# Performance work log

Hardware: AMD Instinct MI355X
Metric: run time of the kernel (lower is better)

## Reference

```python
import jax, jax.numpy as jnp
import numpy as np

DN = ('NCH', 'OIH', 'NCH')  # conv dimension numbers: [batch, channel, length]

def setup_inputs() -> dict:
    key = jax.random.key(0)
    ks = jax.random.split(key, 8)
    B, S, L, D, F, V = 16, 64, 128, 512, 256, 30000
    return {
        'text': jax.random.randint(ks[0], (B, S, L), 0, V),
        'embed': jax.random.normal(ks[1], (V, D), dtype=jnp.float32),
        'w3': jax.random.normal(ks[2], (F, D, 3), dtype=jnp.float32) * 0.05,
        'b3': jax.random.normal(ks[3], (F,), dtype=jnp.float32) * 0.05,
        'w4': jax.random.normal(ks[4], (F, D, 4), dtype=jnp.float32) * 0.05,
        'b4': jax.random.normal(ks[5], (F,), dtype=jnp.float32) * 0.05,
        'w5': jax.random.normal(ks[6], (F, D, 5), dtype=jnp.float32) * 0.05,
        'b5': jax.random.normal(ks[7], (F,), dtype=jnp.float32) * 0.05,
    }

def reference(text, embed, w3, b3, w4, b4, w5, b5):
    B, S, L = text.shape
    # Embed tokens, flatten episodes x utterances into one batch, channels-first.
    x = embed[text]                                   # [B, S, L, D]
    x = x.reshape(B * S, L, -1).transpose(0, 2, 1)    # [BS, D, L]
    outs = []
    for w, b in ((w3, b3), (w4, b4), (w5, b5)):
        y = jax.lax.conv_general_dilated(x, w, (1,), 'VALID', dimension_numbers=DN)
        # max-over-time pooling (valid conv -> length L-K+1)
        outs.append(jnp.max(y + b[None, :, None], axis=2))  # [BS, F]
    out = jax.nn.relu(jnp.concatenate(outs, axis=1))  # [BS, 3F]
    return out.reshape(B, S, -1)
```

## Files before the change

### kernel.cpp

```cpp
#include <hip/hip_runtime.h>
#include <hip/hip_bf16.h>


typedef __bf16 bf16x8 __attribute__((ext_vector_type(8)));
typedef float f32x4 __attribute__((ext_vector_type(4)));

#define XROWS 132
#define XELEMS ((size_t)1024 * XROWS * 512)
#define SLAB_STRIDE 520
#define SLAB_ROWS 133
#define SLAB_BYTES (SLAB_ROWS * SLAB_STRIDE * 2)
#define WQ_ELEMS 1572864

__device__ __forceinline__ void async16(const void* g, void* l) {
    __builtin_amdgcn_global_load_lds(
        (const __attribute__((address_space(1))) void*)g,
        (__attribute__((address_space(3))) void*)l, 16, 0, 0);
}

__global__ void pack_x_kernel(const int* __restrict__ text,
                              const float* __restrict__ embed,
                              __bf16* __restrict__ x) {
    const int tid  = threadIdx.x;
    const int rr   = blockIdx.x * 4 + (tid >> 6);
    const int lane = tid & 63;
    const int bs   = rr / XROWS;
    const int t    = rr - bs * XROWS;
    __bf16* dst = x + (size_t)rr * 512 + lane * 8;
    bf16x8 o = {};
    if (t < 128) {
        const int token = text[bs * 128 + t];
        const float* src = embed + (size_t)token * 512 + lane * 8;
        const float4 v0 = *(const float4*)(src);
        const float4 v1 = *(const float4*)(src + 4);
        o[0] = (__bf16)v0.x; o[1] = (__bf16)v0.y;
        o[2] = (__bf16)v0.z; o[3] = (__bf16)v0.w;
        o[4] = (__bf16)v1.x; o[5] = (__bf16)v1.y;
        o[6] = (__bf16)v1.z; o[7] = (__bf16)v1.w;
    }
    *(bf16x8*)dst = o;
}

__global__ void pack_w_kernel(const float* __restrict__ w3,
                              const float* __restrict__ w4,
                              const float* __restrict__ w5,
                              __bf16* __restrict__ wq) {
    const int t    = blockIdx.x * 256 + threadIdx.x;
    const int g    = t >> 6;
    const int lane = t & 63;
    int rel, Kw; const float* w;
    if (g < 768)       { rel = g;        Kw = 3; w = w3; }
    else if (g < 1792) { rel = g - 768;  Kw = 4; w = w4; }
    else               { rel = g - 1792; Kw = 5; w = w5; }
    const int kq  = rel >> 4;
    const int n16 = rel & 15;
    const int f   = n16 * 16 + (lane & 15);
    const int k0  = kq * 32 + (lane >> 4) * 8;
    const int tap = k0 >> 9;
    const int d0  = k0 & 511;
    const float* src = w + ((size_t)f * 512 + d0) * Kw + tap;
    bf16x8 o;
#pragma unroll
    for (int j = 0; j < 8; ++j) o[j] = (__bf16)src[j * Kw];
    *(bf16x8*)(wq + (size_t)t * 8) = o;
}

__global__ __launch_bounds__(512, 2) void conv_gemm_kernel(
        const __bf16* __restrict__ x,
        const __bf16* __restrict__ wq,
        const float* __restrict__ b3,
        const float* __restrict__ b4,
        const float* __restrict__ b5,
        float* __restrict__ out) {
    extern __shared__ __bf16 slab[];

    const int tid  = threadIdx.x;
    const int wave = tid >> 6;
    const int lane = tid & 63;

    const int lin = blockIdx.x;
    const int xcd = lin & 7;
    const int idx = lin >> 3;
    const int bsh = idx / 3;
    const int c   = idx - bsh * 3;
    const int bs  = bsh * 8 + xcd;
    const int KW  = 3 + c;
    const int nkq = KW << 4;
    const int cbase = (c == 0) ? 0 : (c == 1) ? 393216 : 917504;

    const __bf16* xb = x + (size_t)bs * (XROWS * 512);

    for (int r = wave; r < XROWS; r += 8)
        async16(xb + r * 512 + lane * 8, &slab[r * SLAB_STRIDE]);
    __syncthreads();

    const int wm = wave & 1, wn = wave >> 1;
    const int lm = lane & 15, lk = lane >> 4;

    const __bf16* ap = slab + (wm * 64 + lm) * SLAB_STRIDE + lk * 8;
    const __bf16* bp = wq + cbase + (size_t)(wn * 4) * 512 + lane * 8;

    f32x4 acc[4][4];
#pragma unroll
    for (int i = 0; i < 4; ++i)
#pragma unroll
        for (int j = 0; j < 4; ++j) acc[i][j] = (f32x4){0.f, 0.f, 0.f, 0.f};

    bf16x8 A2[2][4], B4[4][4];

    auto loadB = [&](bf16x8* d, int kb) {
        const __bf16* p = bp + (size_t)kb * 8192;
        d[0] = *(const bf16x8*)(p);
        d[1] = *(const bf16x8*)(p + 512);
        d[2] = *(const bf16x8*)(p + 1024);
        d[3] = *(const bf16x8*)(p + 1536);
    };
    auto mfma16 = [&](const bf16x8* a, const bf16x8* b) {
#pragma unroll
        for (int mt = 0; mt < 4; ++mt)
#pragma unroll
            for (int nt = 0; nt < 4; ++nt)
                acc[mt][nt] = __builtin_amdgcn_mfma_f32_16x16x32_bf16(
                    a[mt], b[nt], acc[mt][nt], 0, 0, 0);
    };

    loadB(B4[0], 0); loadB(B4[1], 1); loadB(B4[2], 2); loadB(B4[3], 3);
#pragma unroll
    for (int mt = 0; mt < 4; ++mt) {
        A2[0][mt] = *(const bf16x8*)(ap + mt * (16 * SLAB_STRIDE));
        A2[1][mt] = *(const bf16x8*)(ap + 32 + mt * (16 * SLAB_STRIDE));
    }

    for (int tap = 0; tap < KW; ++tap) {
        const int kq0 = tap << 4;
#pragma unroll
        for (int q = 0; q < 16; ++q) {
            mfma16(A2[q & 1], B4[q & 3]);
            {
                const int off = (q + 2 < 16) ? (q + 2) * 32
                                             : SLAB_STRIDE + (q - 14) * 32;
#pragma unroll
                for (int mt = 0; mt < 4; ++mt)
                    A2[q & 1][mt] = *(const bf16x8*)
                        (ap + off + mt * (16 * SLAB_STRIDE));
            }
            {
                int kb = kq0 + q + 4;
                kb = (kb < nkq) ? kb : (nkq - 1);
                loadB(B4[q & 3], kb);
            }
        }
        ap += SLAB_STRIDE;
    }

    const int Tv = 126 - c;
    float cmax[4];
#pragma unroll
    for (int nt = 0; nt < 4; ++nt) {
        float mx = -3.0e38f;
#pragma unroll
        for (int mt = 0; mt < 4; ++mt) {
            const int mb = wm * 64 + mt * 16 + lk * 4;
#pragma unroll
            for (int r = 0; r < 4; ++r) {
                const float v = acc[mt][nt][r];
                if (mb + r < Tv) mx = fmaxf(mx, v);
            }
        }
        mx = fmaxf(mx, __shfl_xor(mx, 16, 64));
        mx = fmaxf(mx, __shfl_xor(mx, 32, 64));
        cmax[nt] = mx;
    }
    __syncthreads();
    float* red = (float*)slab;
    if (lk == 0) {
#pragma unroll
        for (int nt = 0; nt < 4; ++nt)
            red[wm * 256 + wn * 64 + nt * 16 + lm] = cmax[nt];
    }
    __syncthreads();
    if (tid < 256) {
        const float* bias = (c == 0) ? b3 : (c == 1) ? b4 : b5;
        float v = fmaxf(red[tid], red[256 + tid]) + bias[tid];
        out[(size_t)bs * 768 + c * 256 + tid] = fmaxf(v, 0.f);
    }
}

extern "C" void kernel_launch(void* const* d_in, const int* in_sizes, int n_in,
                              void* d_out, int out_size, void* d_ws, size_t ws_size,
                              hipStream_t stream) {
    const int*   text  = (const int*)d_in[0];
    const float* embed = (const float*)d_in[1];
    const float* w3    = (const float*)d_in[2];
    const float* b3    = (const float*)d_in[3];
    const float* w4    = (const float*)d_in[4];
    const float* b4    = (const float*)d_in[5];
    const float* w5    = (const float*)d_in[6];
    const float* b5    = (const float*)d_in[7];
    float* out = (float*)d_out;

    __bf16* x  = (__bf16*)d_ws;
    __bf16* wq = x + XELEMS;

    (void)hipFuncSetAttribute((const void*)conv_gemm_kernel,
                              hipFuncAttributeMaxDynamicSharedMemorySize,
                              SLAB_BYTES);

    pack_x_kernel<<<1024 * XROWS / 4, 256, 0, stream>>>(text, embed, x);
    pack_w_kernel<<<768, 256, 0, stream>>>(w3, w4, w5, wq);
    conv_gemm_kernel<<<3072, 512, SLAB_BYTES, stream>>>(x, wq, b3, b4, b5, out);
}
```

Baseline: 514.5 us.

## Fuse embedding gather into conv GEMM with half-depth swizzled LDS slab

Removes the separate pack_x kernel and its bf16 workspace round-trip, so each conv block gathers and converts its own embedding rows straight into LDS. The D dimension is processed in two halves of 256, which shrinks the LDS slab to 132x512 bytes and uses an XOR swizzle in place of padding to avoid bank conflicts. Blocks grow to 1024 threads with a 4x4 wave grid and half the accumulators per wave. In exchange, each embedding row is re-gathered from fp32 three times (once per filter width), and the gather for the second half serialises behind a barrier instead of overlapping with compute.

```diff
diff --git a/kernel.cpp b/kernel.cpp
--- a/kernel.cpp
+++ b/kernel.cpp
@@ -5,41 +5,10 @@
 typedef __bf16 bf16x8 __attribute__((ext_vector_type(8)));
 typedef float f32x4 __attribute__((ext_vector_type(4)));
 
-#define XROWS 132
-#define XELEMS ((size_t)1024 * XROWS * 512)
-#define SLAB_STRIDE 520
-#define SLAB_ROWS 133
-#define SLAB_BYTES (SLAB_ROWS * SLAB_STRIDE * 2)
+#define ROWS 132
+#define ROWB 512
+#define SLAB_BYTES (ROWS * ROWB)
 #define WQ_ELEMS 1572864
-
-__device__ __forceinline__ void async16(const void* g, void* l) {
-    __builtin_amdgcn_global_load_lds(
-        (const __attribute__((address_space(1))) void*)g,
-        (__attribute__((address_space(3))) void*)l, 16, 0, 0);
-}
-
-__global__ void pack_x_kernel(const int* __restrict__ text,
-                              const float* __restrict__ embed,
-                              __bf16* __restrict__ x) {
-    const int tid  = threadIdx.x;
-    const int rr   = blockIdx.x * 4 + (tid >> 6);
-    const int lane = tid & 63;
-    const int bs   = rr / XROWS;
-    const int t    = rr - bs * XROWS;
-    __bf16* dst = x + (size_t)rr * 512 + lane * 8;
-    bf16x8 o = {};
-    if (t < 128) {
-        const int token = text[bs * 128 + t];
-        const float* src = embed + (size_t)token * 512 + lane * 8;
-        const float4 v0 = *(const float4*)(src);
-        const float4 v1 = *(const float4*)(src + 4);
-        o[0] = (__bf16)v0.x; o[1] = (__bf16)v0.y;
-        o[2] = (__bf16)v0.z; o[3] = (__bf16)v0.w;
-        o[4] = (__bf16)v1.x; o[5] = (__bf16)v1.y;
-        o[6] = (__bf16)v1.z; o[7] = (__bf16)v1.w;
-    }
-    *(bf16x8*)dst = o;
-}
 
 __global__ void pack_w_kernel(const float* __restrict__ w3,
                               const float* __restrict__ w4,
@@ -65,14 +34,15 @@
     *(bf16x8*)(wq + (size_t)t * 8) = o;
 }
 
-__global__ __launch_bounds__(512, 2) void conv_gemm_kernel(
-        const __bf16* __restrict__ x,
+__global__ __launch_bounds__(1024, 4) void conv_gemm_kernel(
+        const int* __restrict__ text,
+        const float* __restrict__ embed,
         const __bf16* __restrict__ wq,
         const float* __restrict__ b3,
         const float* __restrict__ b4,
         const float* __restrict__ b5,
         float* __restrict__ out) {
-    extern __shared__ __bf16 slab[];
+    extern __shared__ char slab[];
 
     const int tid  = threadIdx.x;
     const int wave = tid >> 6;
@@ -85,29 +55,21 @@
     const int c   = idx - bsh * 3;
     const int bs  = bsh * 8 + xcd;
     const int KW  = 3 + c;
-    const int nkq = KW << 4;
-    const int cbase = (c == 0) ? 0 : (c == 1) ? 393216 : 917504;
-
-    const __bf16* xb = x + (size_t)bs * (XROWS * 512);
-
-    for (int r = wave; r < XROWS; r += 8)
-        async16(xb + r * 512 + lane * 8, &slab[r * SLAB_STRIDE]);
-    __syncthreads();
-
-    const int wm = wave & 1, wn = wave >> 1;
+    const size_t cbase = (c == 0) ? 0 : (c == 1) ? 393216 : 917504;
+
+    const int wm = wave & 3, wn = wave >> 2;
     const int lm = lane & 15, lk = lane >> 4;
-
-    const __bf16* ap = slab + (wm * 64 + lm) * SLAB_STRIDE + lk * 8;
+    const int ls = lane & 31, lh = lane >> 5;
+
     const __bf16* bp = wq + cbase + (size_t)(wn * 4) * 512 + lane * 8;
 
-    f32x4 acc[4][4];
-#pragma unroll
-    for (int i = 0; i < 4; ++i)
+    f32x4 acc[2][4];
+#pragma unroll
+    for (int i = 0; i < 2; ++i)
 #pragma unroll
         for (int j = 0; j < 4; ++j) acc[i][j] = (f32x4){0.f, 0.f, 0.f, 0.f};
 
-    bf16x8 A2[2][4], B4[4][4];
-
+    bf16x8 B4[2][4];
     auto loadB = [&](bf16x8* d, int kb) {
         const __bf16* p = bp + (size_t)kb * 8192;
         d[0] = *(const bf16x8*)(p);
@@ -115,42 +77,68 @@
         d[2] = *(const bf16x8*)(p + 1024);
         d[3] = *(const bf16x8*)(p + 1536);
     };
-    auto mfma16 = [&](const bf16x8* a, const bf16x8* b) {
-#pragma unroll
-        for (int mt = 0; mt < 4; ++mt)
-#pragma unroll
-            for (int nt = 0; nt < 4; ++nt)
-                acc[mt][nt] = __builtin_amdgcn_mfma_f32_16x16x32_bf16(
-                    a[mt], b[nt], acc[mt][nt], 0, 0, 0);
+    auto mfma8 = [&](const bf16x8 a0, const bf16x8 a1, const bf16x8* b) {
+#pragma unroll
+        for (int nt = 0; nt < 4; ++nt)
+            acc[0][nt] = __builtin_amdgcn_mfma_f32_16x16x32_bf16(
+                a0, b[nt], acc[0][nt], 0, 0, 0);
+#pragma unroll
+        for (int nt = 0; nt < 4; ++nt)
+            acc[1][nt] = __builtin_amdgcn_mfma_f32_16x16x32_bf16(
+                a1, b[nt], acc[1][nt], 0, 0, 0);
     };
 
-    loadB(B4[0], 0); loadB(B4[1], 1); loadB(B4[2], 2); loadB(B4[3], 3);
-#pragma unroll
-    for (int mt = 0; mt < 4; ++mt) {
-        A2[0][mt] = *(const bf16x8*)(ap + mt * (16 * SLAB_STRIDE));
-        A2[1][mt] = *(const bf16x8*)(ap + 32 + mt * (16 * SLAB_STRIDE));
-    }
-
-    for (int tap = 0; tap < KW; ++tap) {
-        const int kq0 = tap << 4;
-#pragma unroll
-        for (int q = 0; q < 16; ++q) {
-            mfma16(A2[q & 1], B4[q & 3]);
-            {
-                const int off = (q + 2 < 16) ? (q + 2) * 32
-                                             : SLAB_STRIDE + (q - 14) * 32;
-#pragma unroll
-                for (int mt = 0; mt < 4; ++mt)
-                    A2[q & 1][mt] = *(const bf16x8*)
-                        (ap + off + mt * (16 * SLAB_STRIDE));
-            }
-            {
-                int kb = kq0 + q + 4;
-                kb = (kb < nkq) ? kb : (nkq - 1);
-                loadB(B4[q & 3], kb);
+    for (int h = 0; h < 2; ++h) {
+        const int kq0   = h * 8;
+        const int maxkq = (KW - 1) * 16 + h * 8 + 7;
+
+        loadB(B4[0], kq0);
+        loadB(B4[1], kq0 + 1);
+
+        if (h) __syncthreads();
+
+#pragma unroll
+        for (int i = 0; i < 5; ++i) {
+            const int r = i * 32 + wave * 2 + lh;
+            if (r < ROWS) {
+                bf16x8 o = {};
+                if (r < 128) {
+                    const int tok = text[bs * 128 + r];
+                    const float* src = embed + (size_t)tok * 512 + h * 256 + ls * 8;
+                    const float4 v0 = *(const float4*)(src);
+                    const float4 v1 = *(const float4*)(src + 4);
+                    o[0] = (__bf16)v0.x; o[1] = (__bf16)v0.y;
+                    o[2] = (__bf16)v0.z; o[3] = (__bf16)v0.w;
+                    o[4] = (__bf16)v1.x; o[5] = (__bf16)v1.y;
+                    o[6] = (__bf16)v1.z; o[7] = (__bf16)v1.w;
+                }
+                *(bf16x8*)(slab + r * ROWB + ((ls * 16) ^ ((r & 7) << 4))) = o;
             }
         }
-        ap += SLAB_STRIDE;
+        __syncthreads();
+
+        for (int tap = 0; tap < KW; ++tap) {
+            int P[2][2];
+#pragma unroll
+            for (int mt = 0; mt < 2; ++mt) {
+                const int row = wm * 32 + mt * 16 + lm + tap;
+                const int x46 = (row & 7) << 4;
+                const int Bb  = row * ROWB + ((lk * 16) ^ (x46 & 48));
+                const int E   = x46 & 64;
+                P[mt][0] = Bb + E;
+                P[mt][1] = Bb + 64 - E;
+            }
+            const int kqt = tap * 16 + h * 8;
+#pragma unroll
+            for (int q = 0; q < 8; ++q) {
+                const bf16x8 a0 = *(const bf16x8*)(slab + P[0][q & 1] + (q >> 1) * 128);
+                const bf16x8 a1 = *(const bf16x8*)(slab + P[1][q & 1] + (q >> 1) * 128);
+                mfma8(a0, a1, B4[q & 1]);
+                int kqn = kqt + ((q < 6) ? (q + 2) : (q + 10));
+                kqn = (kqn <= maxkq) ? kqn : maxkq;
+                loadB(B4[q & 1], kqn);
+            }
+        }
     }
 
     const int Tv = 126 - c;
@@ -159,8 +147,8 @@
     for (int nt = 0; nt < 4; ++nt) {
         float mx = -3.0e38f;
 #pragma unroll
-        for (int mt = 0; mt < 4; ++mt) {
-            const int mb = wm * 64 + mt * 16 + lk * 4;
+        for (int mt = 0; mt < 2; ++mt) {
+            const int mb = wm * 32 + mt * 16 + lk * 4;
 #pragma unroll
             for (int r = 0; r < 4; ++r) {
                 const float v = acc[mt][nt][r];
@@ -181,7 +169,8 @@
     __syncthreads();
     if (tid < 256) {
         const float* bias = (c == 0) ? b3 : (c == 1) ? b4 : b5;
-        float v = fmaxf(red[tid], red[256 + tid]) + bias[tid];
+        float v = fmaxf(fmaxf(red[tid], red[256 + tid]),
+                        fmaxf(red[512 + tid], red[768 + tid])) + bias[tid];
         out[(size_t)bs * 768 + c * 256 + tid] = fmaxf(v, 0.f);
     }
 }
@@ -199,14 +188,13 @@
     const float* b5    = (const float*)d_in[7];
     float* out = (float*)d_out;
 
-    __bf16* x  = (__bf16*)d_ws;
-    __bf16* wq = x + XELEMS;
+    __bf16* wq = (__bf16*)d_ws;
 
     (void)hipFuncSetAttribute((const void*)conv_gemm_kernel,
                               hipFuncAttributeMaxDynamicSharedMemorySize,
                               SLAB_BYTES);
 
-    pack_x_kernel<<<1024 * XROWS / 4, 256, 0, stream>>>(text, embed, x);
     pack_w_kernel<<<768, 256, 0, stream>>>(w3, w4, w5, wq);
-    conv_gemm_kernel<<<3072, 512, SLAB_BYTES, stream>>>(x, wq, b3, b4, b5, out);
+    conv_gemm_kernel<<<3072, 1024, SLAB_BYTES, stream>>>(text, embed, wq,
+                                                         b3, b4, b5, out);
 }
```

New measurement: 576.0 us. 11.9% more time.
